# Kernel tuning notes

Measured on AMD Instinct MI355X. Metric: run time of the kernel, lower is better.

The kernel has to match this reference:

```python
import jax, jax.numpy as jnp
import numpy as np

H = 16        # num_attention_heads
KV = 4        # num_key_value_heads
DH = 128      # head_dim
THETA = 10000.0
MIN_VAL = -1000000000000000.0


def _rope_tables(L):
    # inv_freq: (DH/2,), positions: (L,)
    inv_freq = 1.0 / (THETA ** (jnp.arange(0, DH, 2, dtype=jnp.float32) / DH))
    pos = jnp.arange(L, dtype=jnp.float32)
    freq = pos[:, None] * inv_freq[None, :]          # (L, DH/2)
    emb = jnp.concatenate([freq, freq], axis=-1)      # (L, DH)
    return jnp.cos(emb), jnp.sin(emb)


def _apply_rope(x, cos, sin):
    # x: (B, h, L, DH); cos/sin: (L, DH)
    left = x[..., : DH // 2]
    right = -x[..., DH // 2 :]
    rot = jnp.concatenate([right, left], axis=-1)
    return x * cos[None, None] + rot * sin[None, None]


def setup_inputs() -> dict:
    key = jax.random.key(0)
    ks = jax.random.split(key, 5)
    B, L, D = 2, 2048, 2048
    s = 0.02
    return {
        "hidden_state": jax.random.normal(ks[0], (B, L, D), jnp.float32),
        "attention_mask": jnp.ones((B, L), jnp.int32),
        "Wq": jax.random.normal(ks[1], (H * DH, D), jnp.float32) * s,
        "Wk": jax.random.normal(ks[2], (KV * DH, D), jnp.float32) * s,
        "Wv": jax.random.normal(ks[3], (KV * DH, D), jnp.float32) * s,
        "Wo": jax.random.normal(ks[4], (D, D), jnp.float32) * s,
    }


def reference(hidden_state, attention_mask, Wq, Wk, Wv, Wo):
    B, L, D = hidden_state.shape
    cos, sin = _rope_tables(L)

    q = jnp.einsum('bld,ed->ble', hidden_state, Wq).reshape(B, L, H, DH).transpose(0, 2, 1, 3)
    k = jnp.einsum('bld,ed->ble', hidden_state, Wk).reshape(B, L, KV, DH).transpose(0, 2, 1, 3)
    v = jnp.einsum('bld,ed->ble', hidden_state, Wv).reshape(B, L, KV, DH).transpose(0, 2, 1, 3)

    q = _apply_rope(q, cos, sin)
    k = _apply_rope(k, cos, sin)

    # GQA: repeat each KV head H/KV times -> (B, H, L, DH)
    g = H // KV
    k = jnp.repeat(k, g, axis=1)
    v = jnp.repeat(v, g, axis=1)

    scores = jnp.einsum('bhqd,bhkd->bhqk', q, k) / np.sqrt(DH)  # (B,H,L,L)

    causal = jnp.triu(jnp.full((L, L), MIN_VAL, jnp.float32), k=1)[None, None]  # (1,1,L,L)
    pad = (attention_mask == 0)[:, None, None, :]  # (B,1,1,L)
    mask = jnp.where(pad, MIN_VAL, causal)
    scores = scores + mask

    attn = jax.nn.softmax(scores.astype(jnp.float32), axis=-1).astype(q.dtype)
    out = jnp.einsum('bhqk,bhkd->bhqd', attn, v)
    out = out.transpose(0, 2, 1, 3).reshape(B, L, H * DH)
    return jnp.einsum('ble,de->bld', out, Wo)
```

## Files before the change

### kernel.cpp

```cpp
#include <hip/hip_runtime.h>
#include <cstdint>
#include <cmath>


typedef __bf16 bf16_t;
typedef __bf16 bf16x8 __attribute__((ext_vector_type(8)));
typedef __bf16 bf16x4 __attribute__((ext_vector_type(4)));
typedef float  f32x4  __attribute__((ext_vector_type(4)));

#define HQ   16
#define HKV  4
#define GQA  4
#define DHD  128
#define BB   2
#define LL   2048
#define DDIM 2048
#define MINV (-1e15f)
#define QSC  0.12751744f

static __device__ __forceinline__ f32x4 mfma16(bf16x8 a, bf16x8 b, f32x4 c) {
  return __builtin_amdgcn_mfma_f32_16x16x32_bf16(a, b, c, 0, 0, 0);
}

static __device__ __forceinline__ f32x4 mfma16k16(bf16x4 a, bf16x4 b, f32x4 c) {
#if __has_builtin(__builtin_amdgcn_mfma_f32_16x16x16bf16_1k)
  typedef short s4 __attribute__((ext_vector_type(4)));
  union U { bf16x4 h; s4 s; };
  U ua, ub; ua.h = a; ub.h = b;
  return __builtin_amdgcn_mfma_f32_16x16x16bf16_1k(ua.s, ub.s, c, 0, 0, 0);
#elif __has_builtin(__builtin_amdgcn_mfma_f32_16x16x16_bf16)
  return __builtin_amdgcn_mfma_f32_16x16x16_bf16(a, b, c, 0, 0, 0);
#else
  f32x4 d;
  asm volatile("v_mfma_f32_16x16x16_bf16 %0, %1, %2, %3"
               : "=v"(d) : "v"(a), "v"(b), "v"(c));
  return d;
#endif
}

#if __has_builtin(__builtin_amdgcn_exp2f)
#define EXP2F(x) __builtin_amdgcn_exp2f(x)
#else
#define EXP2F(x) exp2f(x)
#endif

static __device__ __forceinline__ void gld16(const bf16_t* g, bf16_t* l) {
  __builtin_amdgcn_global_load_lds(
      (const __attribute__((address_space(1))) void*)g,
      (__attribute__((address_space(3))) void*)l,
      16, 0, 0);
}

struct CastArgs {
  const float* s[5];
  bf16_t* d[5];
  int n[5];
};

__global__ __launch_bounds__(256) void cast5_kernel(CastArgs a) {
  const int t = blockIdx.y;
  const int i8 = (blockIdx.x * 256 + threadIdx.x) * 8;
  if (i8 >= a.n[t]) return;
  const float4* s = (const float4*)(a.s[t] + i8);
  float4 x = s[0], y = s[1];
  bf16x8 o = {(bf16_t)x.x, (bf16_t)x.y, (bf16_t)x.z, (bf16_t)x.w,
              (bf16_t)y.x, (bf16_t)y.y, (bf16_t)y.z, (bf16_t)y.w};
  *(bf16x8*)(a.d[t] + i8) = o;
}

template <int STORE>
__global__ __launch_bounds__(256) void gemm_tile(const bf16_t* __restrict__ A,
                                                 const bf16_t* __restrict__ W,
                                                 void* __restrict__ C0,
                                                 bf16_t* __restrict__ Ck,
                                                 bf16_t* __restrict__ Cv,
                                                 int M, int N, int K) {
  __shared__ __align__(16) bf16_t As[128 * 32];
  __shared__ __align__(16) bf16_t Bs[128 * 32];
  const int tid  = threadIdx.x;
  const int lane = tid & 63;
  const int wave = tid >> 6;
  const int l15  = lane & 15;
  const int quad = lane >> 4;
  const int m0 = blockIdx.y * 128;
  const int n0 = blockIdx.x * 128;

  const int srow = wave * 32 + (lane >> 2);
  const int scol = (lane & 3) * 8;
  const bf16_t* ag = A + (size_t)(m0 + srow) * K + scol;
  const bf16_t* wg = W + (size_t)(n0 + srow) * K + scol;
  bf16_t* al = As + wave * 1024;
  bf16_t* bl = Bs + wave * 1024;

  const int wm   = (wave >> 1) * 64;
  const int nsel = wave & 1;
  auto colof = [&](int ni) { return ((ni & 1) << 4) + ((ni >> 1) << 6) + (nsel << 5); };

  f32x4 acc[4][4];
#pragma unroll
  for (int mi = 0; mi < 4; mi++)
#pragma unroll
    for (int ni = 0; ni < 4; ni++) acc[mi][ni] = {0.f, 0.f, 0.f, 0.f};

  for (int k0 = 0; k0 < K; k0 += 32) {
    __syncthreads();
    gld16(ag + k0, al);
    gld16(ag + k0 + (size_t)16 * K, al + 512);
    gld16(wg + k0, bl);
    gld16(wg + k0 + (size_t)16 * K, bl + 512);
    __syncthreads();
    bf16x8 af[4], bfr[4];
#pragma unroll
    for (int mi = 0; mi < 4; mi++)
      af[mi] = *(const bf16x8*)(As + (wm + mi * 16 + l15) * 32 + quad * 8);
#pragma unroll
    for (int ni = 0; ni < 4; ni++)
      bfr[ni] = *(const bf16x8*)(Bs + (colof(ni) + l15) * 32 + quad * 8);
#pragma unroll
    for (int mi = 0; mi < 4; mi++)
#pragma unroll
      for (int ni = 0; ni < 4; ni++)
        acc[mi][ni] = mfma16(af[mi], bfr[ni], acc[mi][ni]);
  }

  if (STORE == 2) {
    float* C = (float*)C0;
#pragma unroll
    for (int mi = 0; mi < 4; mi++) {
      const int row = m0 + wm + mi * 16 + quad * 4;
#pragma unroll
      for (int ni = 0; ni < 4; ni++) {
        const int col = n0 + colof(ni) + l15;
#pragma unroll
        for (int i = 0; i < 4; i++)
          C[(size_t)(row + i) * N + col] = acc[mi][ni][i];
      }
    }
  } else {
    if (n0 < 2560) {
      const bool isq = (n0 < 2048);
#pragma unroll
      for (int mi = 0; mi < 4; mi++) {
        const int row = m0 + wm + mi * 16 + quad * 4;
#pragma unroll
        for (int ni2 = 0; ni2 < 2; ni2++) {
          const int dl = (nsel << 5) + (ni2 << 4) + l15;
          const float invf = __expf(-(float)dl * 0.14391156862532788f);
#pragma unroll
          for (int i = 0; i < 4; i++) {
            const int l = (row + i) & (LL - 1);
            float sn, cs;
            __sincosf((float)l * invf, &sn, &cs);
            const float x1 = acc[mi][ni2][i];
            const float x2 = acc[mi][ni2 | 2][i];
            const float out_lo = x1 * cs - x2 * sn;
            const float out_hi = x2 * cs + x1 * sn;
            if (isq) {
              bf16_t* base = (bf16_t*)C0 + (size_t)(row + i) * 2048 + n0;
              base[dl]      = (bf16_t)(out_lo * QSC);
              base[dl + 64] = (bf16_t)(out_hi * QSC);
            } else {
              bf16_t* base = Ck + (size_t)(row + i) * 512 + (n0 - 2048);
              base[dl]      = (bf16_t)out_lo;
              base[dl + 64] = (bf16_t)out_hi;
            }
          }
        }
      }
    } else {
#pragma unroll
      for (int mi = 0; mi < 4; mi++) {
        const int row = m0 + wm + mi * 16 + quad * 4;
        const int b = row >> 11;
        const int l0 = row & (LL - 1);
#pragma unroll
        for (int ni = 0; ni < 4; ni++) {
          const int kvcol = n0 - 2560 + colof(ni) + l15;
          const int kvh = kvcol >> 7, d = kvcol & 127;
          bf16x4 w4 = {(bf16_t)acc[mi][ni][0], (bf16_t)acc[mi][ni][1],
                       (bf16_t)acc[mi][ni][2], (bf16_t)acc[mi][ni][3]};
          *(bf16x4*)(Cv + ((size_t)(b * HKV + kvh) * DHD + d) * LL + l0) = w4;
        }
      }
    }
  }
}

__global__ __launch_bounds__(512, 4) void flash_attn2(const bf16_t* __restrict__ q,
                                                      const bf16_t* __restrict__ k,
                                                      const bf16_t* __restrict__ vt,
                                                      const int* __restrict__ amask,
                                                      bf16_t* __restrict__ o) {
  __shared__ __align__(16) bf16_t Kbuf[2][64 * 128];
  __shared__ __align__(16) bf16_t Vbuf[2][128 * 64];
  __shared__ __align__(16) float  Bb[2048];

  const int tid  = threadIdx.x;
  const int lane = tid & 63;
  const int wave = tid >> 6;
  const int l15  = lane & 15;
  const int quad = lane >> 4;

  const int bi   = blockIdx.x;
  const int half = bi >> 8;
  const int jj   = bi & 255;
  const int cc   = jj >> 5;
  const int c    = half ? (15 - cc) : cc;
  const int bh = jj & 31;
  const int b  = bh >> 4;
  const int h  = bh & 15;
  const int kv = h >> 2;

  const int tile = (wave < 4) ? c : (31 - c);
  const int q0   = tile * 64 + (wave & 3) * 16;
  const int nrounds = 32 - c;

  bf16x8 qf[4];
  {
    const bf16_t* qb = q + ((size_t)(b * LL + q0 + l15)) * (HQ * DHD) + h * DHD + quad * 8;
#pragma unroll
    for (int t = 0; t < 4; t++) qf[t] = *(const bf16x8*)(qb + 32 * t);
  }

  f32x4 acc[8];
#pragma unroll
  for (int mt = 0; mt < 8; mt++) acc[mt] = {0.f, 0.f, 0.f, 0.f};
  float m_i = -1e30f;
  float l_i = 0.f;

  const bf16_t* kg_base = k + ((size_t)(b * LL)) * (HKV * DHD) + kv * DHD;
  const bf16_t* vg_base = vt + ((size_t)(b * HKV + kv) * DHD) * LL;

  {
    int4 am = ((const int4*)(amask + b * LL))[tid];
    f32x4 bv = { am.x ? 0.f : MINV, am.y ? 0.f : MINV,
                 am.z ? 0.f : MINV, am.w ? 0.f : MINV };
    ((f32x4*)Bb)[tid] = bv;
  }

  const int krow = tid >> 4, kch = tid & 15;
  const int vrow = tid >> 3, vch = tid & 7;
  const int vc0  = ((vch >> 2) << 5) + (((vch << 1) & 3) << 3) + (((vch >> 1) & 1) << 2);
  const int vblo = vc0 * 2;
  const int ksw  = (krow & 7) << 4;
  const int vsw  = (vrow & 7) << 4;
  const int rsw  = (l15 & 7) << 4;

  const bf16_t* kg0 = kg_base + (size_t)krow * (HKV * DHD) + kch * 8;
  const bf16_t* vg0 = vg_base + (size_t)vrow * LL + vch * 8;

  bf16x8 kl[2], vl[2];
  auto ISSUE = [&](int j0) {
#pragma unroll
    for (int p = 0; p < 2; p++)
      kl[p] = *(const bf16x8*)(kg0 + (size_t)(j0 + p * 32) * (HKV * DHD));
#pragma unroll
    for (int p = 0; p < 2; p++)
      vl[p] = *(const bf16x8*)(vg0 + j0 + (size_t)p * 64 * LL);
  };
  auto STAGE = [&](int bsel) {
    char* kb = (char*)(&Kbuf[bsel][0]);
    char* vb = (char*)(&Vbuf[bsel][0]);
#pragma unroll
    for (int p = 0; p < 2; p++)
      *(bf16x8*)(kb + (size_t)(krow + p * 32) * 256 + ((kch * 16) ^ ksw)) = kl[p];
#pragma unroll
    for (int p = 0; p < 2; p++) {
      char* vbase = vb + (size_t)(vrow + p * 64) * 128;
      bf16x4 lo4 = __builtin_shufflevector(vl[p], vl[p], 0, 1, 2, 3);
      bf16x4 hi4 = __builtin_shufflevector(vl[p], vl[p], 4, 5, 6, 7);
      *(bf16x4*)(vbase + (vblo ^ vsw)) = lo4;
      *(bf16x4*)(vbase + ((vblo + 16) ^ vsw)) = hi4;
    }
  };

  ISSUE(0);
  STAGE(0);
  __syncthreads();

  int cur = 0;
  for (int r = 0; r < nrounds; r++) {
    const int j0 = r * 64;
    const bool last = (r + 1 >= nrounds);
    if (!last) ISSUE(j0 + 64);

    const bool act = (j0 <= q0 + 15);
    if (act) {
      const char* KbC = (const char*)(&Kbuf[cur][0]);
      const char* VbC = (const char*)(&Vbuf[cur][0]);

      f32x4 s[4];
      __builtin_amdgcn_s_setprio(1);
#pragma unroll
      for (int kt = 0; kt < 4; kt++) {
        const char* kr = KbC + (size_t)(kt * 16 + l15) * 256;
        f32x4 s0 = {0.f, 0.f, 0.f, 0.f};
#pragma unroll
        for (int t = 0; t < 4; t++) {
          bf16x8 kf = *(const bf16x8*)(kr + ((quad * 16 + t * 64) ^ rsw));
          s0 = mfma16(kf, qf[t], s0);
        }
        s[kt] = s0;
      }
      __builtin_amdgcn_s_setprio(0);

      const int qrow = q0 + l15;
      const bool diag = (j0 + 63 > q0);
      float mx = -1e30f;
#pragma unroll
      for (int kt = 0; kt < 4; kt++) {
        f32x4 sv = s[kt];
        f32x4 bv = *(const f32x4*)(&Bb[j0 + kt * 16 + quad * 4]);
#pragma unroll
        for (int i = 0; i < 4; i++) {
          float x = sv[i] + bv[i];
          if (diag) {
            int key = j0 + kt * 16 + quad * 4 + i;
            if (key > qrow) x = MINV;
          }
          sv[i] = x;
          mx = fmaxf(mx, x);
        }
        s[kt] = sv;
      }
      if (!__all(mx <= m_i + 8.0f)) {
        mx = fmaxf(mx, __shfl_xor(mx, 16));
        mx = fmaxf(mx, __shfl_xor(mx, 32));
        const float mn = fmaxf(m_i, mx);
        const float alpha = EXP2F(m_i - mn);
        m_i = mn;
        l_i *= alpha;
#pragma unroll
        for (int mt = 0; mt < 8; mt++) {
          acc[mt][0] *= alpha; acc[mt][1] *= alpha;
          acc[mt][2] *= alpha; acc[mt][3] *= alpha;
        }
      }
      const float mn = m_i;
      float sum = 0.f;
      bf16x4 pf[4];
#pragma unroll
      for (int kt = 0; kt < 4; kt++) {
        f32x4 sv = s[kt];
        bf16x4 p4;
#pragma unroll
        for (int i = 0; i < 4; i++) {
          float pe = EXP2F(sv[i] - mn);
          sum += pe;
          p4[i] = (bf16_t)pe;
        }
        pf[kt] = p4;
      }
      l_i += sum;

      __builtin_amdgcn_s_setprio(1);
#pragma unroll
      for (int mt = 0; mt < 8; mt++) {
        const char* vr = VbC + (size_t)(mt * 16 + l15) * 128;
        bf16x8 v01 = *(const bf16x8*)(vr + ((quad * 16) ^ rsw));
        bf16x8 v23 = *(const bf16x8*)(vr + ((64 + quad * 16) ^ rsw));
        bf16x4 va = __builtin_shufflevector(v01, v01, 0, 1, 2, 3);
        bf16x4 vb = __builtin_shufflevector(v01, v01, 4, 5, 6, 7);
        bf16x4 vc = __builtin_shufflevector(v23, v23, 0, 1, 2, 3);
        bf16x4 vd = __builtin_shufflevector(v23, v23, 4, 5, 6, 7);
        acc[mt] = mfma16k16(va, pf[0], acc[mt]);
        acc[mt] = mfma16k16(vb, pf[1], acc[mt]);
        acc[mt] = mfma16k16(vc, pf[2], acc[mt]);
        acc[mt] = mfma16k16(vd, pf[3], acc[mt]);
      }
      __builtin_amdgcn_s_setprio(0);
    }

    if (!last) {
      STAGE(cur ^ 1);
      __syncthreads();
      cur ^= 1;
    }
  }

  {
    l_i += __shfl_xor(l_i, 16);
    l_i += __shfl_xor(l_i, 32);
    const float invl = 1.0f / l_i;
    bf16_t* ob = o + ((size_t)(b * LL + q0 + l15)) * (HQ * DHD) + h * DHD + quad * 4;
#pragma unroll
    for (int mt = 0; mt < 8; mt++) {
      f32x4 a = acc[mt];
      bf16x4 w = {(bf16_t)(a[0] * invl), (bf16_t)(a[1] * invl),
                  (bf16_t)(a[2] * invl), (bf16_t)(a[3] * invl)};
      *(bf16x4*)(ob + mt * 16) = w;
    }
  }
}

extern "C" void kernel_launch(void* const* d_in, const int* in_sizes, int n_in,
                              void* d_out, int out_size, void* d_ws, size_t ws_size,
                              hipStream_t stream) {
  const float* hidden = (const float*)d_in[0];
  const int*   amask  = (const int*)d_in[1];
  const float* Wq     = (const float*)d_in[2];
  const float* Wk     = (const float*)d_in[3];
  const float* Wv     = (const float*)d_in[4];
  const float* Wo     = (const float*)d_in[5];
  float* out = (float*)d_out;

  const int M = BB * LL;
  const size_t MB = 1u << 20;
  char* ws = (char*)d_ws;
  bf16_t* hid_b   = (bf16_t*)(ws);
  bf16_t* q_ws    = (bf16_t*)(ws + 16 * MB);
  bf16_t* attn_ws = (bf16_t*)(ws + 32 * MB);
  bf16_t* k_ws    = (bf16_t*)(ws + 48 * MB);
  bf16_t* vt_ws   = (bf16_t*)(ws + 52 * MB);
  bf16_t* wqkv_b  = (bf16_t*)(ws + 56 * MB);
  bf16_t* wq_b    = wqkv_b;
  bf16_t* wk_b    = (bf16_t*)(ws + 64 * MB);
  bf16_t* wv_b    = (bf16_t*)(ws + 66 * MB);
  bf16_t* wo_b    = (bf16_t*)(ws + 68 * MB);

  CastArgs ca;
  ca.s[0] = hidden; ca.d[0] = hid_b; ca.n[0] = BB * LL * DDIM;
  ca.s[1] = Wq;     ca.d[1] = wq_b;  ca.n[1] = HQ * DHD * DDIM;
  ca.s[2] = Wk;     ca.d[2] = wk_b;  ca.n[2] = HKV * DHD * DDIM;
  ca.s[3] = Wv;     ca.d[3] = wv_b;  ca.n[3] = HKV * DHD * DDIM;
  ca.s[4] = Wo;     ca.d[4] = wo_b;  ca.n[4] = DDIM * DDIM;
  {
    int maxn = BB * LL * DDIM;
    dim3 g((maxn / 8 + 255) / 256, 5);
    cast5_kernel<<<g, 256, 0, stream>>>(ca);
  }

  gemm_tile<3><<<dim3(3072 / 128, M / 128), 256, 0, stream>>>(
      hid_b, wqkv_b, q_ws, k_ws, vt_ws, M, 3072, DDIM);

  flash_attn2<<<512, 512, 0, stream>>>(q_ws, k_ws, vt_ws, amask, attn_ws);

  gemm_tile<2><<<dim3(DDIM / 128, M / 128), 256, 0, stream>>>(
      attn_ws, wo_b, (void*)out, nullptr, nullptr, M, DDIM, DDIM);
}
```

Baseline: 298.4 us.

## Stage K/V tiles with direct global-to-LDS async loads, simplify V layout

Replaces the register-staged K/V prefetch (global load into registers, then swizzled LDS store after compute) with direct global-to-LDS 16-byte loads (gld16) issued at the start of each round into the alternate buffer. The swizzle moves to the global source address so the LDS layout stays conflict-avoiding. The V tile is no longer permuted at store time, so the PV loop now reads four 8-byte chunks per row instead of two 16-byte reads plus shuffles. This frees VGPRs and removes the LDS-store phase before the barrier, at the cost of more, narrower LDS reads for V. It depends on gld16 and the wave-based destination offsets matching the layout the readers expect.

```diff
diff --git a/kernel.cpp b/kernel.cpp
--- a/kernel.cpp
+++ b/kernel.cpp
@@ -240,49 +240,31 @@
 
   const int krow = tid >> 4, kch = tid & 15;
   const int vrow = tid >> 3, vch = tid & 7;
-  const int vc0  = ((vch >> 2) << 5) + (((vch << 1) & 3) << 3) + (((vch >> 1) & 1) << 2);
-  const int vblo = vc0 * 2;
-  const int ksw  = (krow & 7) << 4;
-  const int vsw  = (vrow & 7) << 4;
   const int rsw  = (l15 & 7) << 4;
 
-  const bf16_t* kg0 = kg_base + (size_t)krow * (HKV * DHD) + kch * 8;
-  const bf16_t* vg0 = vg_base + (size_t)vrow * LL + vch * 8;
-
-  bf16x8 kl[2], vl[2];
-  auto ISSUE = [&](int j0) {
+  const bf16_t* ksrc = kg_base + (size_t)krow * (HKV * DHD) + (kch ^ (krow & 7)) * 8;
+  const bf16_t* vsrc = vg_base + (size_t)vrow * LL + (vch ^ (vrow & 7)) * 8;
+  const int ldst = wave * 512;
+
+  auto STAGE_ASYNC = [&](int j0, int bsel) {
+    bf16_t* kb = &Kbuf[bsel][0] + ldst;
+    bf16_t* vb = &Vbuf[bsel][0] + ldst;
 #pragma unroll
     for (int p = 0; p < 2; p++)
-      kl[p] = *(const bf16x8*)(kg0 + (size_t)(j0 + p * 32) * (HKV * DHD));
+      gld16(ksrc + (size_t)(j0 + p * 32) * (HKV * DHD), kb + p * 4096);
 #pragma unroll
     for (int p = 0; p < 2; p++)
-      vl[p] = *(const bf16x8*)(vg0 + j0 + (size_t)p * 64 * LL);
+      gld16(vsrc + j0 + (size_t)(p * 64) * LL, vb + p * 4096);
   };
-  auto STAGE = [&](int bsel) {
-    char* kb = (char*)(&Kbuf[bsel][0]);
-    char* vb = (char*)(&Vbuf[bsel][0]);
-#pragma unroll
-    for (int p = 0; p < 2; p++)
-      *(bf16x8*)(kb + (size_t)(krow + p * 32) * 256 + ((kch * 16) ^ ksw)) = kl[p];
-#pragma unroll
-    for (int p = 0; p < 2; p++) {
-      char* vbase = vb + (size_t)(vrow + p * 64) * 128;
-      bf16x4 lo4 = __builtin_shufflevector(vl[p], vl[p], 0, 1, 2, 3);
-      bf16x4 hi4 = __builtin_shufflevector(vl[p], vl[p], 4, 5, 6, 7);
-      *(bf16x4*)(vbase + (vblo ^ vsw)) = lo4;
-      *(bf16x4*)(vbase + ((vblo + 16) ^ vsw)) = hi4;
-    }
-  };
-
-  ISSUE(0);
-  STAGE(0);
+
+  STAGE_ASYNC(0, 0);
   __syncthreads();
 
   int cur = 0;
   for (int r = 0; r < nrounds; r++) {
     const int j0 = r * 64;
     const bool last = (r + 1 >= nrounds);
-    if (!last) ISSUE(j0 + 64);
+    if (!last) STAGE_ASYNC(j0 + 64, cur ^ 1);
 
     const bool act = (j0 <= q0 + 15);
     if (act) {
@@ -357,12 +339,10 @@
 #pragma unroll
       for (int mt = 0; mt < 8; mt++) {
         const char* vr = VbC + (size_t)(mt * 16 + l15) * 128;
-        bf16x8 v01 = *(const bf16x8*)(vr + ((quad * 16) ^ rsw));
-        bf16x8 v23 = *(const bf16x8*)(vr + ((64 + quad * 16) ^ rsw));
-        bf16x4 va = __builtin_shufflevector(v01, v01, 0, 1, 2, 3);
-        bf16x4 vb = __builtin_shufflevector(v01, v01, 4, 5, 6, 7);
-        bf16x4 vc = __builtin_shufflevector(v23, v23, 0, 1, 2, 3);
-        bf16x4 vd = __builtin_shufflevector(v23, v23, 4, 5, 6, 7);
+        bf16x4 va = *(const bf16x4*)(vr + ((quad * 8) ^ rsw));
+        bf16x4 vb = *(const bf16x4*)(vr + ((32 + quad * 8) ^ rsw));
+        bf16x4 vc = *(const bf16x4*)(vr + ((64 + quad * 8) ^ rsw));
+        bf16x4 vd = *(const bf16x4*)(vr + ((96 + quad * 8) ^ rsw));
         acc[mt] = mfma16k16(va, pf[0], acc[mt]);
         acc[mt] = mfma16k16(vb, pf[1], acc[mt]);
         acc[mt] = mfma16k16(vc, pf[2], acc[mt]);
@@ -372,7 +352,6 @@
     }
 
     if (!last) {
-      STAGE(cur ^ 1);
       __syncthreads();
       cur ^= 1;
     }
```

Result: slower. 308.2 us (+3.3%).
